# Kernel optimization log

Measured on AMD Instinct MI355X. Metric: run time of the kernel, lower is better.

## Reference

```python
import jax, jax.numpy as jnp
import numpy as np

N_NODES = 100000
NEG_SLOPE = 0.2


def gat_layer(x, src, dst, W, al, ar, b):
    # x: [N, F_in]; src/dst: [E]; W: [F_in, F_out]; al/ar/b: [F_out]
    h = x @ W                                  # [N, F_out]
    el = h @ al                                # [N] per-src attention term
    er = h @ ar                                # [N] per-dst attention term
    e = jax.nn.leaky_relu(el[src] + er[dst], NEG_SLOPE)   # [E]
    # edge softmax over incoming edges of each dst node (numerically stable)
    mx = jax.ops.segment_max(e, dst, num_segments=N_NODES)
    mx = jnp.where(jnp.isfinite(mx), mx, 0.0)  # zero-in-degree guard
    ex = jnp.exp(e - mx[dst])
    denom = jax.ops.segment_sum(ex, dst, num_segments=N_NODES)
    alpha = ex / jnp.maximum(denom[dst], 1e-9)             # [E]
    out = jax.ops.segment_sum(alpha[:, None] * h[src], dst, num_segments=N_NODES)
    return out + b


def setup_inputs() -> dict:
    key = jax.random.key(0)
    ks = jax.random.split(key, 11)
    N, E, F_in, F_h = N_NODES, 1600000, 128, 64
    x = jax.random.normal(ks[0], (N, F_in), dtype=jnp.float32)
    src = jax.random.randint(ks[1], (E,), 0, N, dtype=jnp.int32)
    dst = jax.random.randint(ks[2], (E,), 0, N, dtype=jnp.int32)
    s1 = 1.0 / np.sqrt(F_in)
    s2 = 1.0 / np.sqrt(F_h)
    W1 = jax.random.normal(ks[3], (F_in, F_h), dtype=jnp.float32) * s1
    al1 = jax.random.normal(ks[4], (F_h,), dtype=jnp.float32) * s2
    ar1 = jax.random.normal(ks[5], (F_h,), dtype=jnp.float32) * s2
    b1 = jnp.zeros((F_h,), dtype=jnp.float32)
    W2 = jax.random.normal(ks[6], (F_h, F_h), dtype=jnp.float32) * s2
    al2 = jax.random.normal(ks[7], (F_h,), dtype=jnp.float32) * s2
    ar2 = jax.random.normal(ks[8], (F_h,), dtype=jnp.float32) * s2
    b2 = jnp.zeros((F_h,), dtype=jnp.float32)
    return {"x": x, "src": src, "dst": dst, "W1": W1, "al1": al1, "ar1": ar1,
            "b1": b1, "W2": W2, "al2": al2, "ar2": ar2, "b2": b2}


def reference(x, src, dst, W1, al1, ar1, b1, W2, al2, ar2, b2):
    h = gat_layer(x, src, dst, W1, al1, ar1, b1)   # conv1, head squeezed
    h = jax.nn.relu(h)                              # dropout = identity (eval)
    h = gat_layer(h, src, dst, W2, al2, ar2, b2)   # conv2
    return h
```

## Files before the change

kernel.cpp:

```cpp
#include <hip/hip_runtime.h>
#include <hip/hip_fp16.h>

#define NNODES 100000
#define NEG_SLOPE 0.2f
#define NBK 49
#define BKSHIFT 11
#define BKMASK 2047
#define BCAP 35328
#define B1 4096
#define SLSTRIDE 56

typedef _Float16 f16x8 __attribute__((ext_vector_type(8)));
typedef float f32x4 __attribute__((ext_vector_type(4)));


__global__ void k_init(int* __restrict__ gcur, int* __restrict__ offs, int N, int E) {
    int t = threadIdx.x;
    if (t < NBK) gcur[t] = t * BCAP;
    if (t == NBK) offs[N] = E;
}


__global__ __launch_bounds__(256, 4) void k_gemm1b(
    const float* __restrict__ x, const float* __restrict__ W,
    const float* __restrict__ al, const float* __restrict__ ar,
    __half* __restrict__ h, float* __restrict__ el, float* __restrict__ er,
    int N, int nbBin,
    const int* __restrict__ src, const int* __restrict__ dst,
    int* __restrict__ gcur, int* __restrict__ be, int E) {

    __shared__ float4 SMEM[2048];
    __shared__ int lcnt[NBK], lbase[NBK], lcur[NBK];
    int t = threadIdx.x;

    if ((int)blockIdx.x < nbBin) {
        int base = (int)blockIdx.x * B1;
        if (t < NBK) lcnt[t] = 0;
        __syncthreads();
        int dreg[16];
#pragma unroll
        for (int j = 0; j < 16; ++j) {
            int e = base + j * 256 + t;
            dreg[j] = (e < E) ? dst[e] : -1;
            if (e < E) atomicAdd(&lcnt[dreg[j] >> BKSHIFT], 1);
        }
        __syncthreads();
        if (t < NBK) { lbase[t] = atomicAdd(&gcur[t], lcnt[t]); lcur[t] = 0; }
        __syncthreads();
#pragma unroll
        for (int j = 0; j < 16; ++j) {
            int e = base + j * 256 + t;
            if (e < E) {
                int d = dreg[j];
                int bk = d >> BKSHIFT;
                int p = lbase[bk] + atomicAdd(&lcur[bk], 1);
                be[p] = (src[e] << BKSHIFT) | (d & BKMASK);
            }
        }
        return;
    }

    char* A  = (char*)SMEM;
    char* Bw = (char*)SMEM + 16384;
    int row0 = ((int)blockIdx.x - nbBin) * 64;

    for (int i = t; i < 2048; i += 256) {
        int r = i >> 5, c4 = i & 31;
        int rr = row0 + r; if (rr > N - 1) rr = N - 1;
        float4 v = *(const float4*)(x + (size_t)rr * 128 + c4 * 4);
        int byte = r * 256 + ((c4 * 8) ^ ((r & 7) << 4));
        *(__half2*)(A + byte)     = __floats2half2_rn(v.x, v.y);
        *(__half2*)(A + byte + 4) = __floats2half2_rn(v.z, v.w);
    }
    for (int i = t; i < 2048; i += 256) {
        int k = i >> 4, c4 = (i & 15) * 4;
        float4 v = *(const float4*)(W + k * 64 + c4);
        int kb = k * 2;
        *(__half*)(Bw + (c4 + 0) * 256 + (kb ^ (((c4 + 0) & 7) << 4))) = __float2half(v.x);
        *(__half*)(Bw + (c4 + 1) * 256 + (kb ^ (((c4 + 1) & 7) << 4))) = __float2half(v.y);
        *(__half*)(Bw + (c4 + 2) * 256 + (kb ^ (((c4 + 2) & 7) << 4))) = __float2half(v.z);
        *(__half*)(Bw + (c4 + 3) * 256 + (kb ^ (((c4 + 3) & 7) << 4))) = __float2half(v.w);
    }
    __syncthreads();

    int w = t >> 6, l = t & 63, g = l >> 4, c = l & 15;
    int swz = (c & 7) << 4;
    const char* Ar = A + (w * 16 + c) * 256;

    f32x4 acc[4];
#pragma unroll
    for (int t2 = 0; t2 < 4; ++t2) acc[t2] = (f32x4){0.f, 0.f, 0.f, 0.f};
#pragma unroll
    for (int kk = 0; kk < 4; ++kk) {
        int kb = kk * 64 + g * 16;
        f16x8 av = *(const f16x8*)(Ar + (kb ^ swz));
#pragma unroll
        for (int t2 = 0; t2 < 4; ++t2) {
            f16x8 bv = *(const f16x8*)(Bw + (t2 * 16 + c) * 256 + (kb ^ swz));
            acc[t2] = __builtin_amdgcn_mfma_f32_16x16x32_f16(av, bv, acc[t2], 0, 0, 0);
        }
    }

    float alv[4], arv[4];
#pragma unroll
    for (int t2 = 0; t2 < 4; ++t2) { alv[t2] = al[t2 * 16 + c]; arv[t2] = ar[t2 * 16 + c]; }
#pragma unroll
    for (int r = 0; r < 4; ++r) {
        float e1 = 0.f, e2 = 0.f;
#pragma unroll
        for (int t2 = 0; t2 < 4; ++t2) {
            e1 = fmaf(acc[t2][r], alv[t2], e1);
            e2 = fmaf(acc[t2][r], arv[t2], e2);
        }
#pragma unroll
        for (int o = 1; o < 16; o <<= 1) { e1 += __shfl_xor(e1, o); e2 += __shfl_xor(e2, o); }
        int row = row0 + w * 16 + 4 * g + r;
        if (row < N) {
            if (c == 0) { el[row] = e1; er[row] = e2; }
#pragma unroll
            for (int t2 = 0; t2 < 4; ++t2)
                h[(size_t)row * 64 + t2 * 16 + c] = __float2half(acc[t2][r]);
        }
    }
}


__global__ __launch_bounds__(256) void k_offs(const int* __restrict__ be,
                                              const int* __restrict__ gcur,
                                              int* __restrict__ offs, int N) {
    __shared__ int cnt[2048];
    __shared__ int sb[2][256];
    __shared__ int rbeg;
    int B = blockIdx.x, t = threadIdx.x;
    int mycnt = gcur[B] - B * BCAP;
    int ebase = B * BCAP;

    for (int i = t; i < 2048; i += 256) cnt[i] = 0;
    if (t == 0) rbeg = 0;
    __syncthreads();
    for (int i = t; i < mycnt; i += 256) atomicAdd(&cnt[be[ebase + i] & BKMASK], 1);
    if (t < 64) {
        int v = (t < B) ? gcur[t] - t * BCAP : 0;
#pragma unroll
        for (int o = 32; o; o >>= 1) v += __shfl_xor(v, o);
        if (t == 0) rbeg = v;
    }
    __syncthreads();

    int loc[8], s = 0;
#pragma unroll
    for (int i = 0; i < 8; ++i) { loc[i] = s; s += cnt[8 * t + i]; }
    sb[0][t] = s;
    __syncthreads();
    int pi = 0;
    for (int d = 1; d < 256; d <<= 1) {
        int po = pi ^ 1;
        sb[po][t] = sb[pi][t] + (t >= d ? sb[pi][t - d] : 0);
        pi = po;
        __syncthreads();
    }
    int bas = rbeg + sb[pi][t] - s;

    int node0 = (B << BKSHIFT) + 8 * t;
#pragma unroll
    for (int i = 0; i < 8; ++i) {
        int node = node0 + i;
        if (node < N) offs[node] = bas + loc[i];
    }
}


__global__ __launch_bounds__(256) void k_scat(const int* __restrict__ be,
                                              const int* __restrict__ gcur,
                                              const int* __restrict__ offs,
                                              int* __restrict__ csr, int N) {
    int b = blockIdx.x;
    int B = b % SLSTRIDE, sl = b / SLSTRIDE;
    if (B >= NBK) return;

    __shared__ int cur[256];
    int t = threadIdx.x;
    int mycnt = gcur[B] - B * BCAP;
    int ebase = B * BCAP;
    int node = (B << BKSHIFT) + sl * 256 + t;
    cur[t] = (node < N) ? offs[node] : 0;
    __syncthreads();
    for (int i = t; i < mycnt; i += 256) {
        int v = be[ebase + i];
        int loc = v & BKMASK;
        if ((loc >> 8) == sl) {
            int p = atomicAdd(&cur[loc & 255], 1);
            csr[p] = v >> BKSHIFT;
        }
    }
}


__device__ inline float2 h2_to_f2(float bits) {
    return __half22float2(__builtin_bit_cast(__half2, bits));
}

__device__ float4 agg_node(const __half* __restrict__ h,
                           const float* __restrict__ el, float ern,
                           const int* __restrict__ csr_src,
                           int beg, int deg, int lane, int g, size_t foff) {
    float4 accv = make_float4(0.f, 0.f, 0.f, 0.f);

    if (deg <= 64) {
        int sidx = 0;
        float e = -1e30f;
        if (lane < deg) {
            sidx = csr_src[beg + lane];
            e = el[sidx] + ern;
            e = e > 0.f ? e : NEG_SLOPE * e;
        }
        float m = e;
#pragma unroll
        for (int o = 32; o; o >>= 1) m = fmaxf(m, __shfl_xor(m, o));
        float p = (lane < deg) ? __expf(e - m) : 0.f;
        float s = p;
#pragma unroll
        for (int o = 32; o; o >>= 1) s += __shfl_xor(s, o);
        float a = p * (1.f / fmaxf(s, 1e-9f));

        int iters = (deg + 3) >> 2;
        int quad = iters >> 2;
        int i = g;
        for (int t4 = 0; t4 < quad; ++t4, i += 16) {
            int s0 = __shfl(sidx, i),     s1 = __shfl(sidx, i + 4);
            int s2 = __shfl(sidx, i + 8), s3 = __shfl(sidx, i + 12);
            float w0 = __shfl(a, i),     w1 = __shfl(a, i + 4);
            float w2 = __shfl(a, i + 8), w3 = __shfl(a, i + 12);
            float2 r0 = *(const float2*)(h + (size_t)s0 * 64 + foff);
            float2 r1 = *(const float2*)(h + (size_t)s1 * 64 + foff);
            float2 r2 = *(const float2*)(h + (size_t)s2 * 64 + foff);
            float2 r3 = *(const float2*)(h + (size_t)s3 * 64 + foff);
            float2 f00 = h2_to_f2(r0.x), f01 = h2_to_f2(r0.y);
            float2 f10 = h2_to_f2(r1.x), f11 = h2_to_f2(r1.y);
            float2 f20 = h2_to_f2(r2.x), f21 = h2_to_f2(r2.y);
            float2 f30 = h2_to_f2(r3.x), f31 = h2_to_f2(r3.y);
            accv.x = fmaf(w0, f00.x, accv.x); accv.y = fmaf(w0, f00.y, accv.y);
            accv.z = fmaf(w0, f01.x, accv.z); accv.w = fmaf(w0, f01.y, accv.w);
            accv.x = fmaf(w1, f10.x, accv.x); accv.y = fmaf(w1, f10.y, accv.y);
            accv.z = fmaf(w1, f11.x, accv.z); accv.w = fmaf(w1, f11.y, accv.w);
            accv.x = fmaf(w2, f20.x, accv.x); accv.y = fmaf(w2, f20.y, accv.y);
            accv.z = fmaf(w2, f21.x, accv.z); accv.w = fmaf(w2, f21.y, accv.w);
            accv.x = fmaf(w3, f30.x, accv.x); accv.y = fmaf(w3, f30.y, accv.y);
            accv.z = fmaf(w3, f31.x, accv.z); accv.w = fmaf(w3, f31.y, accv.w);
        }
        int rem = iters & 3;
        for (int rr2 = 0; rr2 < rem; ++rr2, i += 4) {
            int s0 = __shfl(sidx, i);
            float w0 = __shfl(a, i);
            float2 r0 = *(const float2*)(h + (size_t)s0 * 64 + foff);
            float2 f00 = h2_to_f2(r0.x), f01 = h2_to_f2(r0.y);
            accv.x = fmaf(w0, f00.x, accv.x); accv.y = fmaf(w0, f00.y, accv.y);
            accv.z = fmaf(w0, f01.x, accv.z); accv.w = fmaf(w0, f01.y, accv.w);
        }
    } else {
        int end = beg + deg;
        float m = -1e30f;
        for (int i = beg + lane; i < end; i += 64) {
            float e = el[csr_src[i]] + ern;
            e = e > 0.f ? e : NEG_SLOPE * e;
            m = fmaxf(m, e);
        }
#pragma unroll
        for (int o = 32; o; o >>= 1) m = fmaxf(m, __shfl_xor(m, o));
        float s = 0.f;
        for (int i = beg + lane; i < end; i += 64) {
            float e = el[csr_src[i]] + ern;
            e = e > 0.f ? e : NEG_SLOPE * e;
            s += __expf(e - m);
        }
#pragma unroll
        for (int o = 32; o; o >>= 1) s += __shfl_xor(s, o);
        float inv = 1.f / fmaxf(s, 1e-9f);
        for (int i = g; i < deg; i += 4) {
            int s0 = csr_src[beg + i];
            float e = el[s0] + ern;
            e = e > 0.f ? e : NEG_SLOPE * e;
            float w0 = __expf(e - m) * inv;
            float2 r0 = *(const float2*)(h + (size_t)s0 * 64 + foff);
            float2 f00 = h2_to_f2(r0.x), f01 = h2_to_f2(r0.y);
            accv.x = fmaf(w0, f00.x, accv.x); accv.y = fmaf(w0, f00.y, accv.y);
            accv.z = fmaf(w0, f01.x, accv.z); accv.w = fmaf(w0, f01.y, accv.w);
        }
    }

#pragma unroll
    for (int o = 16; o <= 32; o <<= 1) {
        accv.x += __shfl_xor(accv.x, o);
        accv.y += __shfl_xor(accv.y, o);
        accv.z += __shfl_xor(accv.z, o);
        accv.w += __shfl_xor(accv.w, o);
    }
    return accv;
}


__global__ __launch_bounds__(256, 4) void k_aggemm(
    const __half* __restrict__ h, const float* __restrict__ el,
    const float* __restrict__ er, const float* __restrict__ b1,
    const int* __restrict__ offs, const int* __restrict__ csr_src,
    const float* __restrict__ W2, const float* __restrict__ al2,
    const float* __restrict__ ar2,
    __half* __restrict__ h2, float* __restrict__ el2, float* __restrict__ er2,
    int N) {

    __shared__ float4 SMEM[1024];
    char* A  = (char*)SMEM;
    char* Bw = (char*)SMEM + 8192;
    int t = threadIdx.x;
    int w = t >> 6, lane = t & 63, g = lane >> 4, fl = lane & 15;
    int row0 = blockIdx.x * 64;

    for (int i = t; i < 1024; i += 256) {
        int k = i >> 4, c4 = (i & 15) * 4;
        float4 v = *(const float4*)(W2 + k * 64 + c4);
        int kb = k * 2;
        *(__half*)(Bw + (c4 + 0) * 128 + (kb ^ (((c4 + 0) & 7) << 4))) = __float2half(v.x);
        *(__half*)(Bw + (c4 + 1) * 128 + (kb ^ (((c4 + 1) & 7) << 4))) = __float2half(v.y);
        *(__half*)(Bw + (c4 + 2) * 128 + (kb ^ (((c4 + 2) & 7) << 4))) = __float2half(v.z);
        *(__half*)(Bw + (c4 + 3) * 128 + (kb ^ (((c4 + 3) & 7) << 4))) = __float2half(v.w);
    }

    const size_t foff = 4 * (size_t)fl;
    float4 bv = *(const float4*)(b1 + foff);
    for (int j = 0; j < 16; ++j) {
        int r = w * 16 + j;
        int n = row0 + r;
        int beg = 0, deg = 0;
        float ern = 0.f;
        if (n < N) {
            beg = offs[n];
            deg = offs[n + 1] - beg;
            ern = er[n];
        }
        float4 accv = agg_node(h, el, ern, csr_src, beg, deg, lane, g, foff);
        if (lane < 16) {
            float ox = fmaxf(accv.x + bv.x, 0.f);
            float oy = fmaxf(accv.y + bv.y, 0.f);
            float oz = fmaxf(accv.z + bv.z, 0.f);
            float ow = fmaxf(accv.w + bv.w, 0.f);
            __half2 h01 = __floats2half2_rn(ox, oy);
            __half2 h23 = __floats2half2_rn(oz, ow);
            float2 pk;
            pk.x = __builtin_bit_cast(float, h01);
            pk.y = __builtin_bit_cast(float, h23);
            *(float2*)(A + r * 128 + ((int)(fl * 8) ^ ((r & 7) << 4))) = pk;
        }
    }
    __syncthreads();

    int c = fl;
    int swz = (c & 7) << 4;
    const char* Ar = A + (w * 16 + c) * 128;

    f32x4 acc[4];
#pragma unroll
    for (int t2 = 0; t2 < 4; ++t2) acc[t2] = (f32x4){0.f, 0.f, 0.f, 0.f};
#pragma unroll
    for (int kk = 0; kk < 2; ++kk) {
        int kb = kk * 64 + g * 16;
        f16x8 av = *(const f16x8*)(Ar + (kb ^ swz));
#pragma unroll
        for (int t2 = 0; t2 < 4; ++t2) {
            f16x8 bvf = *(const f16x8*)(Bw + (t2 * 16 + c) * 128 + (kb ^ swz));
            acc[t2] = __builtin_amdgcn_mfma_f32_16x16x32_f16(av, bvf, acc[t2], 0, 0, 0);
        }
    }

    float alv[4], arv[4];
#pragma unroll
    for (int t2 = 0; t2 < 4; ++t2) { alv[t2] = al2[t2 * 16 + c]; arv[t2] = ar2[t2 * 16 + c]; }
#pragma unroll
    for (int r = 0; r < 4; ++r) {
        float e1 = 0.f, e2 = 0.f;
#pragma unroll
        for (int t2 = 0; t2 < 4; ++t2) {
            e1 = fmaf(acc[t2][r], alv[t2], e1);
            e2 = fmaf(acc[t2][r], arv[t2], e2);
        }
#pragma unroll
        for (int o = 1; o < 16; o <<= 1) { e1 += __shfl_xor(e1, o); e2 += __shfl_xor(e2, o); }
        int row = row0 + w * 16 + 4 * g + r;
        if (row < N) {
            if (c == 0) { el2[row] = e1; er2[row] = e2; }
#pragma unroll
            for (int t2 = 0; t2 < 4; ++t2)
                h2[(size_t)row * 64 + t2 * 16 + c] = __float2half(acc[t2][r]);
        }
    }
}


__global__ __launch_bounds__(256) void k_agg2(const __half* __restrict__ h,
                                              const float* __restrict__ el,
                                              const float* __restrict__ er,
                                              const float* __restrict__ b,
                                              const int* __restrict__ offs,
                                              const int* __restrict__ csr_src,
                                              float* __restrict__ out, int N) {
    int wave = threadIdx.x >> 6, lane = threadIdx.x & 63;
    int n = blockIdx.x * 4 + wave;
    if (n >= N) return;

    int beg = offs[n], deg = offs[n + 1] - beg;
    int g = lane >> 4, fl = lane & 15;
    const size_t foff = 4 * (size_t)fl;

    float4 accv = agg_node(h, el, er[n], csr_src, beg, deg, lane, g, foff);

    if (lane < 16) {
        float4 bv = *(const float4*)(b + foff);
        *(float4*)(out + (size_t)n * 64 + foff) =
            make_float4(accv.x + bv.x, accv.y + bv.y, accv.z + bv.z, accv.w + bv.w);
    }
}


extern "C" void kernel_launch(void* const* d_in, const int* in_sizes, int n_in,
                              void* d_out, int out_size, void* d_ws, size_t ws_size,
                              hipStream_t stream) {
    const float* x   = (const float*)d_in[0];
    const int*   src = (const int*)d_in[1];
    const int*   dst = (const int*)d_in[2];
    const float* W1  = (const float*)d_in[3];
    const float* al1 = (const float*)d_in[4];
    const float* ar1 = (const float*)d_in[5];
    const float* b1  = (const float*)d_in[6];
    const float* W2  = (const float*)d_in[7];
    const float* al2 = (const float*)d_in[8];
    const float* ar2 = (const float*)d_in[9];
    const float* b2  = (const float*)d_in[10];
    float* out = (float*)d_out;

    const int N = NNODES;
    const int E = in_sizes[1];

    __half* h    = (__half*)d_ws;
    __half* h2   = h + (size_t)N * 64;
    int*    be   = (int*)(h2 + (size_t)N * 64);
    int*    csr  = be + (size_t)NBK * BCAP;
    float*  el   = (float*)(csr + E);
    float*  er   = el + N;
    float*  el2  = er + N;
    float*  er2  = el2 + N;
    int*    offs = (int*)(er2 + N);
    int*    gcur = offs + N + 1;

    int nbBin = (E + B1 - 1) / B1;
    int nbG   = (N + 63) / 64;
    int nbR   = (N + 3) / 4;

    k_init<<<1, 64, 0, stream>>>(gcur, offs, N, E);
    k_gemm1b<<<nbBin + nbG, 256, 0, stream>>>(x, W1, al1, ar1, h, el, er, N,
                                              nbBin, src, dst, gcur, be, E);
    k_offs<<<NBK, 256, 0, stream>>>(be, gcur, offs, N);
    k_scat<<<8 * SLSTRIDE, 256, 0, stream>>>(be, gcur, offs, csr, N);
    k_aggemm<<<nbG, 256, 0, stream>>>(h, el, er, b1, offs, csr,
                                      W2, al2, ar2, h2, el2, er2, N);
    k_agg2<<<nbR, 256, 0, stream>>>(h2, el2, er2, b2, offs, csr, out, N);
}
```

Baseline: 203.2 us.

## Aggregate two nodes per wave and pre-swizzle weights once in init

After: 207.7 us. 2.2% more time.

```diff
diff --git a/kernel.cpp b/kernel.cpp
--- a/kernel.cpp
+++ b/kernel.cpp
@@ -14,15 +14,29 @@
 typedef float f32x4 __attribute__((ext_vector_type(4)));
 
 
-__global__ void k_init(int* __restrict__ gcur, int* __restrict__ offs, int N, int E) {
-    int t = threadIdx.x;
-    if (t < NBK) gcur[t] = t * BCAP;
-    if (t == NBK) offs[N] = E;
-}
-
-
-__global__ __launch_bounds__(256, 4) void k_gemm1b(
-    const float* __restrict__ x, const float* __restrict__ W,
+__global__ void k_init(const float* __restrict__ W1, const float* __restrict__ W2,
+                       __half* __restrict__ Wt1, __half* __restrict__ Wt2,
+                       int* __restrict__ gcur, int* __restrict__ offs, int N, int E) {
+    int t = threadIdx.x, b = blockIdx.x;
+    if (b == 0) {
+        if (t < NBK) gcur[t] = t * BCAP;
+        if (t == NBK) offs[N] = E;
+    }
+    char* w1b = (char*)Wt1;
+    for (int i = b * 1024 + t; i < (b + 1) * 1024 && i < 8192; i += 256) {
+        int k = i >> 6, c = i & 63;
+        *(__half*)(w1b + c * 256 + ((2 * k) ^ ((c & 7) << 4))) = __float2half(W1[i]);
+    }
+    char* w2b = (char*)Wt2;
+    for (int i = b * 512 + t; i < (b + 1) * 512 && i < 4096; i += 256) {
+        int k = i >> 6, c = i & 63;
+        *(__half*)(w2b + c * 128 + ((2 * k) ^ ((c & 7) << 4))) = __float2half(W2[i]);
+    }
+}
+
+
+__global__ __launch_bounds__(256, 5) void k_gemm1b(
+    const float* __restrict__ x, const __half* __restrict__ Wt1,
     const float* __restrict__ al, const float* __restrict__ ar,
     __half* __restrict__ h, float* __restrict__ el, float* __restrict__ er,
     int N, int nbBin,
@@ -72,15 +86,8 @@
         *(__half2*)(A + byte)     = __floats2half2_rn(v.x, v.y);
         *(__half2*)(A + byte + 4) = __floats2half2_rn(v.z, v.w);
     }
-    for (int i = t; i < 2048; i += 256) {
-        int k = i >> 4, c4 = (i & 15) * 4;
-        float4 v = *(const float4*)(W + k * 64 + c4);
-        int kb = k * 2;
-        *(__half*)(Bw + (c4 + 0) * 256 + (kb ^ (((c4 + 0) & 7) << 4))) = __float2half(v.x);
-        *(__half*)(Bw + (c4 + 1) * 256 + (kb ^ (((c4 + 1) & 7) << 4))) = __float2half(v.y);
-        *(__half*)(Bw + (c4 + 2) * 256 + (kb ^ (((c4 + 2) & 7) << 4))) = __float2half(v.z);
-        *(__half*)(Bw + (c4 + 3) * 256 + (kb ^ (((c4 + 3) & 7) << 4))) = __float2half(v.w);
-    }
+    for (int i = t; i < 1024; i += 256)
+        ((float4*)Bw)[i] = ((const float4*)Wt1)[i];
     __syncthreads();
 
     int w = t >> 6, l = t & 63, g = l >> 4, c = l & 15;
@@ -200,94 +207,43 @@
     return __half22float2(__builtin_bit_cast(__half2, bits));
 }
 
+__device__ inline void edge_one(float2 r0, float w0, float4& accv) {
+    float2 f00 = h2_to_f2(r0.x), f01 = h2_to_f2(r0.y);
+    accv.x = fmaf(w0, f00.x, accv.x); accv.y = fmaf(w0, f00.y, accv.y);
+    accv.z = fmaf(w0, f01.x, accv.z); accv.w = fmaf(w0, f01.y, accv.w);
+}
+
 __device__ float4 agg_node(const __half* __restrict__ h,
                            const float* __restrict__ el, float ern,
                            const int* __restrict__ csr_src,
                            int beg, int deg, int lane, int g, size_t foff) {
     float4 accv = make_float4(0.f, 0.f, 0.f, 0.f);
-
-    if (deg <= 64) {
-        int sidx = 0;
-        float e = -1e30f;
-        if (lane < deg) {
-            sidx = csr_src[beg + lane];
-            e = el[sidx] + ern;
-            e = e > 0.f ? e : NEG_SLOPE * e;
-        }
-        float m = e;
-#pragma unroll
-        for (int o = 32; o; o >>= 1) m = fmaxf(m, __shfl_xor(m, o));
-        float p = (lane < deg) ? __expf(e - m) : 0.f;
-        float s = p;
-#pragma unroll
-        for (int o = 32; o; o >>= 1) s += __shfl_xor(s, o);
-        float a = p * (1.f / fmaxf(s, 1e-9f));
-
-        int iters = (deg + 3) >> 2;
-        int quad = iters >> 2;
-        int i = g;
-        for (int t4 = 0; t4 < quad; ++t4, i += 16) {
-            int s0 = __shfl(sidx, i),     s1 = __shfl(sidx, i + 4);
-            int s2 = __shfl(sidx, i + 8), s3 = __shfl(sidx, i + 12);
-            float w0 = __shfl(a, i),     w1 = __shfl(a, i + 4);
-            float w2 = __shfl(a, i + 8), w3 = __shfl(a, i + 12);
-            float2 r0 = *(const float2*)(h + (size_t)s0 * 64 + foff);
-            float2 r1 = *(const float2*)(h + (size_t)s1 * 64 + foff);
-            float2 r2 = *(const float2*)(h + (size_t)s2 * 64 + foff);
-            float2 r3 = *(const float2*)(h + (size_t)s3 * 64 + foff);
-            float2 f00 = h2_to_f2(r0.x), f01 = h2_to_f2(r0.y);
-            float2 f10 = h2_to_f2(r1.x), f11 = h2_to_f2(r1.y);
-            float2 f20 = h2_to_f2(r2.x), f21 = h2_to_f2(r2.y);
-            float2 f30 = h2_to_f2(r3.x), f31 = h2_to_f2(r3.y);
-            accv.x = fmaf(w0, f00.x, accv.x); accv.y = fmaf(w0, f00.y, accv.y);
-            accv.z = fmaf(w0, f01.x, accv.z); accv.w = fmaf(w0, f01.y, accv.w);
-            accv.x = fmaf(w1, f10.x, accv.x); accv.y = fmaf(w1, f10.y, accv.y);
-            accv.z = fmaf(w1, f11.x, accv.z); accv.w = fmaf(w1, f11.y, accv.w);
-            accv.x = fmaf(w2, f20.x, accv.x); accv.y = fmaf(w2, f20.y, accv.y);
-            accv.z = fmaf(w2, f21.x, accv.z); accv.w = fmaf(w2, f21.y, accv.w);
-            accv.x = fmaf(w3, f30.x, accv.x); accv.y = fmaf(w3, f30.y, accv.y);
-            accv.z = fmaf(w3, f31.x, accv.z); accv.w = fmaf(w3, f31.y, accv.w);
-        }
-        int rem = iters & 3;
-        for (int rr2 = 0; rr2 < rem; ++rr2, i += 4) {
-            int s0 = __shfl(sidx, i);
-            float w0 = __shfl(a, i);
-            float2 r0 = *(const float2*)(h + (size_t)s0 * 64 + foff);
-            float2 f00 = h2_to_f2(r0.x), f01 = h2_to_f2(r0.y);
-            accv.x = fmaf(w0, f00.x, accv.x); accv.y = fmaf(w0, f00.y, accv.y);
-            accv.z = fmaf(w0, f01.x, accv.z); accv.w = fmaf(w0, f01.y, accv.w);
-        }
-    } else {
-        int end = beg + deg;
-        float m = -1e30f;
-        for (int i = beg + lane; i < end; i += 64) {
-            float e = el[csr_src[i]] + ern;
-            e = e > 0.f ? e : NEG_SLOPE * e;
-            m = fmaxf(m, e);
-        }
-#pragma unroll
-        for (int o = 32; o; o >>= 1) m = fmaxf(m, __shfl_xor(m, o));
-        float s = 0.f;
-        for (int i = beg + lane; i < end; i += 64) {
-            float e = el[csr_src[i]] + ern;
-            e = e > 0.f ? e : NEG_SLOPE * e;
-            s += __expf(e - m);
-        }
-#pragma unroll
-        for (int o = 32; o; o >>= 1) s += __shfl_xor(s, o);
-        float inv = 1.f / fmaxf(s, 1e-9f);
-        for (int i = g; i < deg; i += 4) {
-            int s0 = csr_src[beg + i];
-            float e = el[s0] + ern;
-            e = e > 0.f ? e : NEG_SLOPE * e;
-            float w0 = __expf(e - m) * inv;
-            float2 r0 = *(const float2*)(h + (size_t)s0 * 64 + foff);
-            float2 f00 = h2_to_f2(r0.x), f01 = h2_to_f2(r0.y);
-            accv.x = fmaf(w0, f00.x, accv.x); accv.y = fmaf(w0, f00.y, accv.y);
-            accv.z = fmaf(w0, f01.x, accv.z); accv.w = fmaf(w0, f01.y, accv.w);
-        }
-    }
-
+    int end = beg + deg;
+    float m = -1e30f;
+    for (int i = beg + lane; i < end; i += 64) {
+        float e = el[csr_src[i]] + ern;
+        e = e > 0.f ? e : NEG_SLOPE * e;
+        m = fmaxf(m, e);
+    }
+#pragma unroll
+    for (int o = 32; o; o >>= 1) m = fmaxf(m, __shfl_xor(m, o));
+    float s = 0.f;
+    for (int i = beg + lane; i < end; i += 64) {
+        float e = el[csr_src[i]] + ern;
+        e = e > 0.f ? e : NEG_SLOPE * e;
+        s += __expf(e - m);
+    }
+#pragma unroll
+    for (int o = 32; o; o >>= 1) s += __shfl_xor(s, o);
+    float inv = 1.f / fmaxf(s, 1e-9f);
+    for (int i = g; i < deg; i += 4) {
+        int s0 = csr_src[beg + i];
+        float e = el[s0] + ern;
+        e = e > 0.f ? e : NEG_SLOPE * e;
+        float w0 = __expf(e - m) * inv;
+        float2 r0 = *(const float2*)(h + (size_t)s0 * 64 + foff);
+        edge_one(r0, w0, accv);
+    }
 #pragma unroll
     for (int o = 16; o <= 32; o <<= 1) {
         accv.x += __shfl_xor(accv.x, o);
@@ -298,12 +254,101 @@
     return accv;
 }
 
-
-__global__ __launch_bounds__(256, 4) void k_aggemm(
+__device__ void agg_node2(const __half* __restrict__ h,
+                          const float* __restrict__ el,
+                          float ernA, float ernB,
+                          const int* __restrict__ csr_src,
+                          int begA, int degA, int begB, int degB,
+                          int lane, int g, size_t foff,
+                          float4& accA, float4& accB) {
+    accA = make_float4(0.f, 0.f, 0.f, 0.f);
+    accB = make_float4(0.f, 0.f, 0.f, 0.f);
+
+    if (degA > 64 || degB > 64) {
+        accA = agg_node(h, el, ernA, csr_src, begA, degA, lane, g, foff);
+        accB = agg_node(h, el, ernB, csr_src, begB, degB, lane, g, foff);
+        return;
+    }
+
+    int sA = 0, sB = 0;
+    float eA = -1e30f, eB = -1e30f;
+    if (lane < degA) {
+        sA = csr_src[begA + lane];
+        float v = el[sA] + ernA;
+        eA = v > 0.f ? v : NEG_SLOPE * v;
+    }
+    if (lane < degB) {
+        sB = csr_src[begB + lane];
+        float v = el[sB] + ernB;
+        eB = v > 0.f ? v : NEG_SLOPE * v;
+    }
+    float mA = eA, mB = eB;
+#pragma unroll
+    for (int o = 32; o; o >>= 1) {
+        mA = fmaxf(mA, __shfl_xor(mA, o));
+        mB = fmaxf(mB, __shfl_xor(mB, o));
+    }
+    float pA = (lane < degA) ? __expf(eA - mA) : 0.f;
+    float pB = (lane < degB) ? __expf(eB - mB) : 0.f;
+    float uA = pA, uB = pB;
+#pragma unroll
+    for (int o = 32; o; o >>= 1) {
+        uA += __shfl_xor(uA, o);
+        uB += __shfl_xor(uB, o);
+    }
+    float aA = pA * (1.f / fmaxf(uA, 1e-9f));
+    float aB = pB * (1.f / fmaxf(uB, 1e-9f));
+
+    int nqA = (degA + 3) >> 2, nqB = (degB + 3) >> 2;
+    int nq = nqA > nqB ? nqA : nqB;
+    int oct = nq >> 2, rem = nq & 3;
+    int i = g;
+    for (int t4 = 0; t4 < oct; ++t4, i += 16) {
+        int a0 = __shfl(sA, i),      a1 = __shfl(sA, i + 4);
+        int a2 = __shfl(sA, i + 8),  a3 = __shfl(sA, i + 12);
+        int b0 = __shfl(sB, i),      b1 = __shfl(sB, i + 4);
+        int b2 = __shfl(sB, i + 8),  b3 = __shfl(sB, i + 12);
+        float wa0 = __shfl(aA, i),     wa1 = __shfl(aA, i + 4);
+        float wa2 = __shfl(aA, i + 8), wa3 = __shfl(aA, i + 12);
+        float wb0 = __shfl(aB, i),     wb1 = __shfl(aB, i + 4);
+        float wb2 = __shfl(aB, i + 8), wb3 = __shfl(aB, i + 12);
+        float2 ra0 = *(const float2*)(h + (size_t)a0 * 64 + foff);
+        float2 ra1 = *(const float2*)(h + (size_t)a1 * 64 + foff);
+        float2 ra2 = *(const float2*)(h + (size_t)a2 * 64 + foff);
+        float2 ra3 = *(const float2*)(h + (size_t)a3 * 64 + foff);
+        float2 rb0 = *(const float2*)(h + (size_t)b0 * 64 + foff);
+        float2 rb1 = *(const float2*)(h + (size_t)b1 * 64 + foff);
+        float2 rb2 = *(const float2*)(h + (size_t)b2 * 64 + foff);
+        float2 rb3 = *(const float2*)(h + (size_t)b3 * 64 + foff);
+        edge_one(ra0, wa0, accA); edge_one(ra1, wa1, accA);
+        edge_one(ra2, wa2, accA); edge_one(ra3, wa3, accA);
+        edge_one(rb0, wb0, accB); edge_one(rb1, wb1, accB);
+        edge_one(rb2, wb2, accB); edge_one(rb3, wb3, accB);
+    }
+    for (; rem > 0; --rem, i += 4) {
+        int a0 = __shfl(sA, i), b0 = __shfl(sB, i);
+        float wa0 = __shfl(aA, i), wb0 = __shfl(aB, i);
+        float2 ra0 = *(const float2*)(h + (size_t)a0 * 64 + foff);
+        float2 rb0 = *(const float2*)(h + (size_t)b0 * 64 + foff);
+        edge_one(ra0, wa0, accA);
+        edge_one(rb0, wb0, accB);
+    }
+
+#pragma unroll
+    for (int o = 16; o <= 32; o <<= 1) {
+        accA.x += __shfl_xor(accA.x, o); accA.y += __shfl_xor(accA.y, o);
+        accA.z += __shfl_xor(accA.z, o); accA.w += __shfl_xor(accA.w, o);
+        accB.x += __shfl_xor(accB.x, o); accB.y += __shfl_xor(accB.y, o);
+        accB.z += __shfl_xor(accB.z, o); accB.w += __shfl_xor(accB.w, o);
+    }
+}
+
+
+__global__ __launch_bounds__(256, 6) void k_aggemm(
     const __half* __restrict__ h, const float* __restrict__ el,
     const float* __restrict__ er, const float* __restrict__ b1,
     const int* __restrict__ offs, const int* __restrict__ csr_src,
-    const float* __restrict__ W2, const float* __restrict__ al2,
+    const __half* __restrict__ Wt2, const float* __restrict__ al2,
     const float* __restrict__ ar2,
     __half* __restrict__ h2, float* __restrict__ el2, float* __restrict__ er2,
     int N) {
@@ -315,40 +360,38 @@
     int w = t >> 6, lane = t & 63, g = lane >> 4, fl = lane & 15;
     int row0 = blockIdx.x * 64;
 
-    for (int i = t; i < 1024; i += 256) {
-        int k = i >> 4, c4 = (i & 15) * 4;
-        float4 v = *(const float4*)(W2 + k * 64 + c4);
-        int kb = k * 2;
-        *(__half*)(Bw + (c4 + 0) * 128 + (kb ^ (((c4 + 0) & 7) << 4))) = __float2half(v.x);
-        *(__half*)(Bw + (c4 + 1) * 128 + (kb ^ (((c4 + 1) & 7) << 4))) = __float2half(v.y);
-        *(__half*)(Bw + (c4 + 2) * 128 + (kb ^ (((c4 + 2) & 7) << 4))) = __float2half(v.z);
-        *(__half*)(Bw + (c4 + 3) * 128 + (kb ^ (((c4 + 3) & 7) << 4))) = __float2half(v.w);
-    }
+    for (int i = t; i < 512; i += 256)
+        ((float4*)Bw)[i] = ((const float4*)Wt2)[i];
 
     const size_t foff = 4 * (size_t)fl;
     float4 bv = *(const float4*)(b1 + foff);
-    for (int j = 0; j < 16; ++j) {
-        int r = w * 16 + j;
-        int n = row0 + r;
-        int beg = 0, deg = 0;
-        float ern = 0.f;
-        if (n < N) {
-            beg = offs[n];
-            deg = offs[n + 1] - beg;
-            ern = er[n];
-        }
-        float4 accv = agg_node(h, el, ern, csr_src, beg, deg, lane, g, foff);
+    for (int j = 0; j < 16; j += 2) {
+        int rA = w * 16 + j;
+        int nA = row0 + rA, nB = nA + 1;
+        int begA = 0, degA = 0, begB = 0, degB = 0;
+        float ernA = 0.f, ernB = 0.f;
+        if (nA < N) { begA = offs[nA]; degA = offs[nA + 1] - begA; ernA = er[nA]; }
+        if (nB < N) { begB = offs[nB]; degB = offs[nB + 1] - begB; ernB = er[nB]; }
+        float4 accA, accB;
+        agg_node2(h, el, ernA, ernB, csr_src, begA, degA, begB, degB,
+                  lane, g, foff, accA, accB);
         if (lane < 16) {
-            float ox = fmaxf(accv.x + bv.x, 0.f);
-            float oy = fmaxf(accv.y + bv.y, 0.f);
-            float oz = fmaxf(accv.z + bv.z, 0.f);
-            float ow = fmaxf(accv.w + bv.w, 0.f);
-            __half2 h01 = __floats2half2_rn(ox, oy);
-            __half2 h23 = __floats2half2_rn(oz, ow);
+            float ox = fmaxf(accA.x + bv.x, 0.f);
+            float oy = fmaxf(accA.y + bv.y, 0.f);
+            float oz = fmaxf(accA.z + bv.z, 0.f);
+            float ow = fmaxf(accA.w + bv.w, 0.f);
             float2 pk;
-            pk.x = __builtin_bit_cast(float, h01);
-            pk.y = __builtin_bit_cast(float, h23);
-            *(float2*)(A + r * 128 + ((int)(fl * 8) ^ ((r & 7) << 4))) = pk;
+            pk.x = __builtin_bit_cast(float, __floats2half2_rn(ox, oy));
+            pk.y = __builtin_bit_cast(float, __floats2half2_rn(oz, ow));
+            *(float2*)(A + rA * 128 + ((int)(fl * 8) ^ ((rA & 7) << 4))) = pk;
+            int rB = rA + 1;
+            ox = fmaxf(accB.x + bv.x, 0.f);
+            oy = fmaxf(accB.y + bv.y, 0.f);
+            oz = fmaxf(accB.z + bv.z, 0.f);
+            ow = fmaxf(accB.w + bv.w, 0.f);
+            pk.x = __builtin_bit_cast(float, __floats2half2_rn(ox, oy));
+            pk.y = __builtin_bit_cast(float, __floats2half2_rn(oz, ow));
+            *(float2*)(A + rB * 128 + ((int)(fl * 8) ^ ((rB & 7) << 4))) = pk;
         }
     }
     __syncthreads();
@@ -395,27 +438,38 @@
 }
 
 
-__global__ __launch_bounds__(256) void k_agg2(const __half* __restrict__ h,
-                                              const float* __restrict__ el,
-                                              const float* __restrict__ er,
-                                              const float* __restrict__ b,
-                                              const int* __restrict__ offs,
-                                              const int* __restrict__ csr_src,
-                                              float* __restrict__ out, int N) {
+__global__ __launch_bounds__(256, 6) void k_agg2(const __half* __restrict__ h,
+                                                 const float* __restrict__ el,
+                                                 const float* __restrict__ er,
+                                                 const float* __restrict__ b,
+                                                 const int* __restrict__ offs,
+                                                 const int* __restrict__ csr_src,
+                                                 float* __restrict__ out, int N) {
     int wave = threadIdx.x >> 6, lane = threadIdx.x & 63;
-    int n = blockIdx.x * 4 + wave;
-    if (n >= N) return;
-
-    int beg = offs[n], deg = offs[n + 1] - beg;
+    int nA = blockIdx.x * 8 + wave * 2;
+    if (nA >= N) return;
+    int nB = nA + 1;
+
     int g = lane >> 4, fl = lane & 15;
     const size_t foff = 4 * (size_t)fl;
 
-    float4 accv = agg_node(h, el, er[n], csr_src, beg, deg, lane, g, foff);
+    int begA = offs[nA], degA = offs[nA + 1] - begA;
+    float ernA = er[nA];
+    int begB = 0, degB = 0;
+    float ernB = 0.f;
+    if (nB < N) { begB = offs[nB]; degB = offs[nB + 1] - begB; ernB = er[nB]; }
+
+    float4 accA, accB;
+    agg_node2(h, el, ernA, ernB, csr_src, begA, degA, begB, degB,
+              lane, g, foff, accA, accB);
 
     if (lane < 16) {
         float4 bv = *(const float4*)(b + foff);
-        *(float4*)(out + (size_t)n * 64 + foff) =
-            make_float4(accv.x + bv.x, accv.y + bv.y, accv.z + bv.z, accv.w + bv.w);
+        *(float4*)(out + (size_t)nA * 64 + foff) =
+            make_float4(accA.x + bv.x, accA.y + bv.y, accA.z + bv.z, accA.w + bv.w);
+        if (nB < N)
+            *(float4*)(out + (size_t)nB * 64 + foff) =
+                make_float4(accB.x + bv.x, accB.y + bv.y, accB.z + bv.z, accB.w + bv.w);
     }
 }
 
@@ -449,17 +503,19 @@
     float*  er2  = el2 + N;
     int*    offs = (int*)(er2 + N);
     int*    gcur = offs + N + 1;
+    __half* Wt1  = (__half*)(gcur + NBK + 15);
+    __half* Wt2  = Wt1 + 8192;
 
     int nbBin = (E + B1 - 1) / B1;
     int nbG   = (N + 63) / 64;
-    int nbR   = (N + 3) / 4;
-
-    k_init<<<1, 64, 0, stream>>>(gcur, offs, N, E);
-    k_gemm1b<<<nbBin + nbG, 256, 0, stream>>>(x, W1, al1, ar1, h, el, er, N,
+    int nbR2  = (N + 7) / 8;
+
+    k_init<<<8, 256, 0, stream>>>(W1, W2, Wt1, Wt2, gcur, offs, N, E);
+    k_gemm1b<<<nbBin + nbG, 256, 0, stream>>>(x, Wt1, al1, ar1, h, el, er, N,
                                               nbBin, src, dst, gcur, be, E);
     k_offs<<<NBK, 256, 0, stream>>>(be, gcur, offs, N);
     k_scat<<<8 * SLSTRIDE, 256, 0, stream>>>(be, gcur, offs, csr, N);
     k_aggemm<<<nbG, 256, 0, stream>>>(h, el, er, b1, offs, csr,
-                                      W2, al2, ar2, h2, el2, er2, N);
-    k_agg2<<<nbR, 256, 0, stream>>>(h2, el2, er2, b2, offs, csr, out, N);
-}
+                                      Wt2, al2, ar2, h2, el2, er2, N);
+    k_agg2<<<nbR2, 256, 0, stream>>>(h2, el2, er2, b2, offs, csr, out, N);
+}
```
